# Performance work log

Measured on AMD Instinct MI355X. Metric: run time of the kernel, lower is better.

Reference implementation:

```python
import jax, jax.numpy as jnp
import numpy as np

N_E = 8192
E_DIM = 256
BETA = 0.25


def setup_inputs() -> dict:
    key = jax.random.key(0)
    k1, k2 = jax.random.split(key)
    z = jax.random.normal(k1, (16, E_DIM, 32, 32), dtype=jnp.float32)
    # matches torch init: uniform(-1/n_e, 1/n_e)
    emb_w = jax.random.uniform(k2, (N_E, E_DIM), dtype=jnp.float32,
                               minval=-1.0 / N_E, maxval=1.0 / N_E)
    return {"z": z, "emb_w": emb_w}


def reference(z, emb_w):
    B, C, H, W = z.shape
    zt = jnp.transpose(z, (0, 2, 3, 1))          # b h w c
    zf = zt.reshape(-1, C)                        # [N, e_dim]
    # d[n, k] = ||zf_n||^2 + ||e_k||^2 - 2 zf_n . e_k
    d = (jnp.sum(zf * zf, axis=1, keepdims=True)
         + jnp.sum(emb_w * emb_w, axis=1)
         - 2.0 * jnp.einsum('bd,nd->bn', zf, emb_w))
    idx = jnp.argmin(d, axis=1)                   # [N]
    z_q = emb_w[idx].reshape(zt.shape)            # b h w c
    sg = jax.lax.stop_gradient
    # legacy=True loss
    loss = jnp.mean((sg(z_q) - zt) ** 2) + BETA * jnp.mean((z_q - sg(zt)) ** 2)
    # straight-through estimator
    z_q_st = zt + sg(z_q - zt)
    z_q_out = jnp.transpose(z_q_st, (0, 3, 1, 2))  # b c h w
    return z_q_out, loss, idx.reshape(B, H, W)
```

## Files before the change

### kernel.cpp

```cpp
#include <hip/hip_runtime.h>
#include <math.h>

typedef unsigned int uint;
typedef unsigned short ushort;
typedef unsigned long long u64;
typedef __attribute__((ext_vector_type(8))) short short8;
typedef __attribute__((ext_vector_type(4))) float f32x4;

#define WS_ZPK  0ull
#define WS_EPK  8388608ull
#define WS_SUMZ 12582912ull
#define WS_GMAX 12648448ull
#define WS_CMAX 46202880ull
#define WS_BEST 50397184ull
#define WS_LOSS 50462720ull

#define DOT_MARGIN 1.5e-4f

__device__ __forceinline__ ushort f2bf(float f) {
  uint b = __float_as_uint(f);
  b += 0x7fffu + ((b >> 16) & 1u);
  return (ushort)(b >> 16);
}
__device__ __forceinline__ uint ford(float f) {
  uint b = __float_as_uint(f);
  return (b & 0x80000000u) ? ~b : (b | 0x80000000u);
}
__device__ __forceinline__ void gload_lds16(const void* g, void* l) {
  __builtin_amdgcn_global_load_lds(
      (const __attribute__((address_space(1))) unsigned int*)g,
      (__attribute__((address_space(3))) unsigned int*)l, 16, 0, 0);
}

__global__ __launch_bounds__(256) void prep_all(const float* __restrict__ z,
                                                const float* __restrict__ emb,
                                                ushort* __restrict__ zpk,
                                                ushort* __restrict__ epk,
                                                float* __restrict__ sumz) {
  __shared__ float tile[64][65];
  const int bidg = blockIdx.x;
  const int t = threadIdx.x;
  if (bidg < 1024) {
    const int bid = bidg;
    const int kt = bid & 3, hwt = (bid >> 2) & 15, b = bid >> 6;
    const int lane = t & 63, grp = t >> 6;
    const float* src = z + b * 262144 + (kt * 64) * 1024 + hwt * 64;
    for (int kk = grp; kk < 64; kk += 4)
      tile[kk][lane] = src[kk * 1024 + lane];
    __syncthreads();
    for (int u = t; u < 512; u += 256) {
      const int n_loc = u & 63, kg = u >> 6;
      const int n = b * 1024 + hwt * 64 + n_loc;
      const int k0 = kt * 64 + kg * 8;
      short8 s;
#pragma unroll
      for (int j = 0; j < 8; ++j) s[j] = (short)f2bf(tile[kg * 8 + j][n_loc]);
      *(short8*)(zpk + (size_t)(n >> 4) * 4096 + (k0 >> 5) * 512 +
                 ((k0 >> 3) & 3) * 128 + (n & 15) * 8) = s;
    }
  } else if (bidg < 2048) {
    const int u = (bidg - 1024) * 256 + t;
    const int c = u >> 5, k0 = (u & 31) * 8;
    const float4 v0 = *(const float4*)(emb + c * 256 + k0);
    const float4 v1 = *(const float4*)(emb + c * 256 + k0 + 4);
    short8 s;
    s[0] = (short)f2bf(v0.x); s[1] = (short)f2bf(v0.y);
    s[2] = (short)f2bf(v0.z); s[3] = (short)f2bf(v0.w);
    s[4] = (short)f2bf(v1.x); s[5] = (short)f2bf(v1.y);
    s[6] = (short)f2bf(v1.z); s[7] = (short)f2bf(v1.w);
    *(short8*)(epk + (size_t)(c >> 4) * 4096 + (k0 >> 5) * 512 +
               ((k0 >> 3) & 3) * 128 + (c & 15) * 8) = s;
  } else {
    const int n = ((bidg - 2048) << 8) + t;
    const int b = n >> 10, hw = n & 1023;
    const float* zb = z + b * 262144 + hw;
    float s = 0.f;
#pragma unroll 8
    for (int c = 0; c < 256; ++c) { const float v = zb[c << 10]; s += v * v; }
    sumz[n] = s;
  }
}

__global__ __launch_bounds__(256) void gemm_screen(const ushort* __restrict__ zpk,
                                                   const ushort* __restrict__ epk,
                                                   uint* __restrict__ gmax,
                                                   ushort* __restrict__ cmax,
                                                   int boff) {
  __shared__ ushort Cs[16384];
  const int t = threadIdx.x;
  const int w = t >> 6, lane = t & 63;
  const int bid = blockIdx.x + boff;
  const int x = bid & 7, y = bid >> 3;
  const int yyv = y & 15;
  const int colb = yyv * 8 + x;
  const int rowg = y >> 4;
  const int n0 = rowg << 10;
  const int m16 = lane & 15, q = lane >> 4;
  const int cix = x * 64 + yyv * 4 + q;

#pragma unroll
  for (int f2 = 0; f2 < 8; ++f2) {
    const int f = w * 8 + f2;
    gload_lds16(epk + (size_t)colb * 16384 + f * 512 + lane * 8, (char*)Cs + f * 1024);
  }

  const ushort* zw = zpk + ((size_t)(n0 >> 4) + w * 4) * 4096 + lane * 8;

  short8 zf[32][4];
#pragma unroll
  for (int v = 0; v < 3; ++v)
#pragma unroll
    for (int jr = 0; jr < 4; ++jr)
      zf[v][jr] = *(const short8*)(zw + ((size_t)((v >> 3) * 16 + jr)) * 4096 +
                                   (v & 7) * 512);
  __syncthreads();

#pragma unroll
  for (int strip = 0; strip < 4; ++strip) {
    const int rbase = n0 + strip * 256 + w * 64;
    f32x4 acc[4][4];
#pragma unroll
    for (int i = 0; i < 4; ++i)
#pragma unroll
      for (int j = 0; j < 4; ++j) acc[i][j] = {0.f, 0.f, 0.f, 0.f};

#pragma unroll
    for (int s32 = 0; s32 < 8; ++s32) {
      const int v = strip * 8 + s32;
      if (v + 3 < 32) {
        const int u = v + 3;
#pragma unroll
        for (int jr = 0; jr < 4; ++jr)
          zf[u][jr] = *(const short8*)(zw + ((size_t)((u >> 3) * 16 + jr)) * 4096 +
                                       (u & 7) * 512);
      }
      short8 cv[4];
#pragma unroll
      for (int ic = 0; ic < 4; ++ic)
        cv[ic] = *(const short8*)&Cs[(size_t)(ic * 8 + s32) * 512 + lane * 8];
#pragma unroll
      for (int ic = 0; ic < 4; ++ic)
#pragma unroll
        for (int jr = 0; jr < 4; ++jr)
          acc[ic][jr] = __builtin_amdgcn_mfma_f32_16x16x32_bf16(cv[ic], zf[v][jr],
                                                                acc[ic][jr], 0, 0, 0);
    }

#pragma unroll
    for (int jr = 0; jr < 4; ++jr) {
      uint pk[4];
      float pm = -INFINITY;
#pragma unroll
      for (int ic = 0; ic < 4; ++ic) {
        float m = fmaxf(fmaxf(acc[ic][jr][0], acc[ic][jr][1]),
                        fmaxf(acc[ic][jr][2], acc[ic][jr][3]));
        m = fmaxf(m, __shfl_xor(m, 16, 64));
        const float o = __shfl_xor(m, 32, 64);
        pm = fmaxf(pm, fmaxf(m, o));
        const float glo = (q & 2) ? o : m;
        const float ghi = (q & 2) ? m : o;
        pk[ic] = (uint)f2bf(glo) | ((uint)f2bf(ghi) << 16);
      }
      const uint sv = (q == 0) ? pk[0] : (q == 1) ? pk[1] : (q == 2) ? pk[2] : pk[3];
      const int row = rbase + jr * 16 + m16;
      gmax[(size_t)row * 512 + cix] = sv;
      if (q == 0) cmax[(size_t)row * 128 + x * 16 + yyv] = f2bf(pm);
    }
  }
}

__global__ __launch_bounds__(1024) void select_rescore(const uint* __restrict__ gmax,
                                                       const ushort* __restrict__ cmax,
                                                       const float* __restrict__ z,
                                                       const float* __restrict__ emb,
                                                       const float* __restrict__ sumz,
                                                       uint* __restrict__ bestI) {
  const int t = threadIdx.x, w = t >> 6, lane = t & 63;
  const int n0 = blockIdx.x << 4;
  const int n = n0 + w;
  __shared__ float zrow[16][260];
  __shared__ ushort hits[16][64];
  const int b_i = n0 >> 10, hw0 = n0 & 1023;
  const float* zb = z + b_i * 262144 + hw0;
#pragma unroll
  for (int i = 0; i < 4; ++i) {
    const int u = t + i * 1024;
    const int c = u >> 4, r = u & 15;
    zrow[r][c] = zb[c * 1024 + r];
  }
  __syncthreads();

  const uint cu = ((const uint*)cmax)[(size_t)n * 64 + lane];
  const float c0 = __uint_as_float(cu << 16);
  const float c1 = __uint_as_float(cu & 0xffff0000u);
  float m = fmaxf(c0, c1);
#pragma unroll
  for (int off = 1; off < 64; off <<= 1) m = fmaxf(m, __shfl_xor(m, off, 64));
  const float thr = m - DOT_MARGIN;

  u64 m0 = __ballot(c0 >= thr);
  u64 m1 = __ballot(c1 >= thr);
  int nh = 0;
  while (m0 | m1) {
    int p;
    if (m0) { const int s = (int)__builtin_ctzll(m0); m0 &= m0 - 1; p = s * 2; }
    else    { const int s = (int)__builtin_ctzll(m1); m1 &= m1 - 1; p = s * 2 + 1; }
    const int xx = p >> 4, yy = p & 15;
    const int cb = (yy * 8 + xx) * 64;
    const uint4 fw = *(const uint4*)(gmax + (size_t)n * 512 + xx * 64 + yy * 4);
    const uint fq[4] = {fw.x, fw.y, fw.z, fw.w};
#pragma unroll
    for (int qq = 0; qq < 4; ++qq) {
      if (__uint_as_float(fq[qq] << 16) >= thr && nh < 64)
        hits[w][nh++] = (ushort)(cb + qq * 16);
      if (__uint_as_float(fq[qq] & 0xffff0000u) >= thr && nh < 64)
        hits[w][nh++] = (ushort)(cb + qq * 16 + 8);
    }
  }
  __threadfence_block();
  const int K = nh;
  const float sz = sumz[n];
  u64 bk = ~0ull;
  for (int id = lane; id < K * 8; id += 64) {
    const int c = hits[w][id >> 3] + (id & 7);
    const float4* ea = (const float4*)(emb + c * 256);
    const float4* za = (const float4*)&zrow[w][0];
    float sdot = 0.f, se = 0.f;
#pragma unroll 8
    for (int k = 0; k < 64; ++k) {
      const float4 a = za[k], e = ea[k];
      sdot = fmaf(a.x, e.x, sdot); sdot = fmaf(a.y, e.y, sdot);
      sdot = fmaf(a.z, e.z, sdot); sdot = fmaf(a.w, e.w, sdot);
      se = fmaf(e.x, e.x, se); se = fmaf(e.y, e.y, se);
      se = fmaf(e.z, e.z, se); se = fmaf(e.w, e.w, se);
    }
    const float d = (sz + se) - 2.f * sdot;
    const u64 key = ((u64)ford(d) << 32) | (uint)c;
    if (key < bk) bk = key;
  }
#pragma unroll
  for (int off = 1; off < 64; off <<= 1) {
    const u64 o = (((u64)(uint)__shfl_xor((int)(bk >> 32), off, 64)) << 32) |
                  (uint)__shfl_xor((int)(bk & 0xffffffffu), off, 64);
    if (o < bk) bk = o;
  }
  if (lane == 0) bestI[n] = (uint)(bk & 0xffffffffu);
}

__global__ __launch_bounds__(256) void gather_kernel(const float* __restrict__ z,
                                                     const float* __restrict__ emb,
                                                     const uint* __restrict__ bestI,
                                                     float* __restrict__ out,
                                                     double* __restrict__ loss_acc,
                                                     uint* __restrict__ done) {
  const int t = threadIdx.x;
  const int n0 = blockIdx.x << 6;
  const int n = n0 + (t & 63);
  const int idx = (int)bestI[n];
  const int b_i = n >> 10, hw = n & 1023;
  const int c0 = t >> 6;
  const float* zb = z + b_i * 262144 + hw;
  float* ob = out + b_i * 262144 + hw;
  const float* eb = emb + idx * 256;
  float lsum = 0.f;
#pragma unroll 4
  for (int c = c0; c < 256; c += 4) {
    const float ev = eb[c];
    const float zv = zb[c << 10];
    ob[c << 10] = ev;
    const float d = ev - zv;
    lsum += d * d;
  }
  if (c0 == 0) out[4194305 + n] = (float)idx;
#pragma unroll
  for (int off = 32; off; off >>= 1) lsum += __shfl_down(lsum, off, 64);
  __shared__ double wsum[4];
  if ((t & 63) == 0) wsum[t >> 6] = (double)lsum;
  __syncthreads();
  if (t == 0) {
    atomicAdd(loss_acc, wsum[0] + wsum[1] + wsum[2] + wsum[3]);
    __threadfence();
    if (atomicAdd(done, 1u) == 255u) {
      __threadfence();
      out[4194304] = (float)(1.25 * (*(volatile double*)loss_acc) / 4194304.0);
    }
  }
}

extern "C" void kernel_launch(void* const* d_in, const int* in_sizes, int n_in,
                              void* d_out, int out_size, void* d_ws, size_t ws_size,
                              hipStream_t stream) {
  const float* z = (const float*)d_in[0];
  const float* emb = (const float*)d_in[1];
  float* out = (float*)d_out;
  char* ws = (char*)d_ws;
  ushort* zpk = (ushort*)(ws + WS_ZPK);
  ushort* epk = (ushort*)(ws + WS_EPK);
  float* sumz = (float*)(ws + WS_SUMZ);
  uint* gmax = (uint*)(ws + WS_GMAX);
  ushort* cmax = (ushort*)(ws + WS_CMAX);
  uint* bestI = (uint*)(ws + WS_BEST);
  double* loss_acc = (double*)(ws + WS_LOSS);
  uint* done = (uint*)(ws + WS_LOSS + 8);

  hipMemsetAsync(ws + WS_LOSS, 0, 16, stream);
  prep_all<<<2112, 256, 0, stream>>>(z, emb, zpk, epk, sumz);
  gemm_screen<<<1024, 256, 0, stream>>>(zpk, epk, gmax, cmax, 0);
  gemm_screen<<<1024, 256, 0, stream>>>(zpk, epk, gmax, cmax, 1024);
  select_rescore<<<1024, 1024, 0, stream>>>(gmax, cmax, z, emb, sumz, bestI);
  gather_kernel<<<256, 256, 0, stream>>>(z, emb, bestI, out, loss_acc, done);
}
```

Baseline: 248.8 us.

## Pool rescore candidates across all warps in select_rescore block

Each row's candidate list is now written into a shared pool for the whole block instead of being rescored by that row's own wavefront. All 1024 threads then split the combined candidate set, and per-row minima are reduced with shared-memory 64-bit atomicMin. This is meant to fix load imbalance when some rows have many candidates and others very few. In exchange it adds extra block barriers, shared-memory atomics, and a prefix sum over the per-row hit counts.

```diff
diff --git a/kernel.cpp b/kernel.cpp
--- a/kernel.cpp
+++ b/kernel.cpp
@@ -180,6 +180,10 @@
   const int n = n0 + w;
   __shared__ float zrow[16][260];
   __shared__ ushort hits[16][64];
+  __shared__ int nhs[16];
+  __shared__ float szs[16];
+  __shared__ u64 rmin[16];
+  __shared__ uint pool[1024];
   const int b_i = n0 >> 10, hw0 = n0 & 1023;
   const float* zb = z + b_i * 262144 + hw0;
 #pragma unroll
@@ -188,7 +192,7 @@
     const int c = u >> 4, r = u & 15;
     zrow[r][c] = zb[c * 1024 + r];
   }
-  __syncthreads();
+  if (t < 16) { szs[t] = sumz[n0 + t]; rmin[t] = ~0ull; }
 
   const uint cu = ((const uint*)cmax)[(size_t)n * 64 + lane];
   const float c0 = __uint_as_float(cu << 16);
@@ -217,34 +221,41 @@
         hits[w][nh++] = (ushort)(cb + qq * 16 + 8);
     }
   }
-  __threadfence_block();
-  const int K = nh;
-  const float sz = sumz[n];
-  u64 bk = ~0ull;
-  for (int id = lane; id < K * 8; id += 64) {
-    const int c = hits[w][id >> 3] + (id & 7);
+  if (lane == 0) nhs[w] = nh;
+  __syncthreads();
+
+  int off = 0, total = 0;
+#pragma unroll
+  for (int ww = 0; ww < 16; ++ww) {
+    const int v = nhs[ww];
+    off += (ww < w) ? v : 0;
+    total += v;
+  }
+  if (lane < nh) pool[off + lane] = ((uint)w << 13) | (uint)hits[w][lane];
+  __syncthreads();
+
+  const int T = total * 8;
+  for (int id = t; id < T; id += 1024) {
+    const uint e = pool[id >> 3];
+    const int r = (int)(e >> 13);
+    const int c = (int)(e & 8191u) + (id & 7);
     const float4* ea = (const float4*)(emb + c * 256);
-    const float4* za = (const float4*)&zrow[w][0];
+    const float4* za = (const float4*)&zrow[r][0];
     float sdot = 0.f, se = 0.f;
 #pragma unroll 8
     for (int k = 0; k < 64; ++k) {
-      const float4 a = za[k], e = ea[k];
-      sdot = fmaf(a.x, e.x, sdot); sdot = fmaf(a.y, e.y, sdot);
-      sdot = fmaf(a.z, e.z, sdot); sdot = fmaf(a.w, e.w, sdot);
-      se = fmaf(e.x, e.x, se); se = fmaf(e.y, e.y, se);
-      se = fmaf(e.z, e.z, se); se = fmaf(e.w, e.w, se);
-    }
-    const float d = (sz + se) - 2.f * sdot;
+      const float4 a = za[k], e4 = ea[k];
+      sdot = fmaf(a.x, e4.x, sdot); sdot = fmaf(a.y, e4.y, sdot);
+      sdot = fmaf(a.z, e4.z, sdot); sdot = fmaf(a.w, e4.w, sdot);
+      se = fmaf(e4.x, e4.x, se); se = fmaf(e4.y, e4.y, se);
+      se = fmaf(e4.z, e4.z, se); se = fmaf(e4.w, e4.w, se);
+    }
+    const float d = (szs[r] + se) - 2.f * sdot;
     const u64 key = ((u64)ford(d) << 32) | (uint)c;
-    if (key < bk) bk = key;
-  }
-#pragma unroll
-  for (int off = 1; off < 64; off <<= 1) {
-    const u64 o = (((u64)(uint)__shfl_xor((int)(bk >> 32), off, 64)) << 32) |
-                  (uint)__shfl_xor((int)(bk & 0xffffffffu), off, 64);
-    if (o < bk) bk = o;
-  }
-  if (lane == 0) bestI[n] = (uint)(bk & 0xffffffffu);
+    atomicMin(&rmin[r], key);
+  }
+  __syncthreads();
+  if (t < 16) bestI[n0 + t] = (uint)(rmin[t] & 0xffffffffu);
 }
 
 __global__ __launch_bounds__(256) void gather_kernel(const float* __restrict__ z,
```

Result: faster. 232.8 us (-6.4%).
